# Kernel optimization log

Measured on AMD Instinct MI355X. Metric: run time of the kernel, lower is better.

The kernel has to match this reference:

```python
import jax, jax.numpy as jnp
import numpy as np

B, T, N, F, H, E = 8, 16, 10000, 64, 64, 1000000
M = B * N  # flattened node count per timestep
NUM_CLASSES = 3


def setup_inputs() -> dict:
    key = jax.random.key(0)
    ks = jax.random.split(key, 10)
    s = 1.0 / np.sqrt(H)
    return {
        "graph_seq": jax.random.normal(ks[0], (B, T, N, F), dtype=jnp.float32),
        "edge_index_seq": jax.random.randint(ks[1], (T, 2, E), 0, M, dtype=jnp.int32),
        "W_gcn": jax.random.normal(ks[2], (F, H), dtype=jnp.float32) / np.sqrt(F),
        "b_gcn": jnp.zeros((H,), dtype=jnp.float32),
        "W_ih": jax.random.uniform(ks[3], (4 * H, H), jnp.float32, -s, s),
        "W_hh": jax.random.uniform(ks[4], (4 * H, H), jnp.float32, -s, s),
        "b_ih": jax.random.uniform(ks[5], (4 * H,), jnp.float32, -s, s),
        "b_hh": jax.random.uniform(ks[6], (4 * H,), jnp.float32, -s, s),
        "W_fc": jax.random.uniform(ks[7], (NUM_CLASSES, H), jnp.float32, -s, s),
        "b_fc": jax.random.uniform(ks[8], (NUM_CLASSES,), jnp.float32, -s, s),
    }


def _forward(graph_seq, edge_index_seq, W_gcn, b_gcn, W_ih, W_hh, b_ih, b_hh, W_fc, b_fc):
    # GCNConv: x' = D^{-1/2}(A+I)D^{-1/2} (x W) + b, applied on flattened (B*N) nodes per timestep.
    xw = jnp.einsum('btnf,fh->btnh', graph_seq, W_gcn)        # [B,T,N,H]
    xw_t = xw.transpose(1, 0, 2, 3).reshape(T, M, H)          # [T, B*N, H], node index = b*N + n

    def gcn_step(_, inp):
        x, ei = inp                                           # x: [M,H], ei: [2,E]
        src, dst = ei[0], ei[1]
        deg = jax.ops.segment_sum(jnp.ones((E,), x.dtype), dst, num_segments=M) + 1.0  # +1 self loop
        dinv = jax.lax.rsqrt(deg)
        coef = dinv[src] * dinv[dst]                          # [E]
        agg = jax.ops.segment_sum(x[src] * coef[:, None], dst, num_segments=M)
        out = agg + x * (dinv * dinv)[:, None] + b_gcn        # self-loop term + bias
        pooled = out.reshape(B, N, H).mean(axis=1)            # mean over nodes -> [B,H]
        return None, pooled

    _, pooled_seq = jax.lax.scan(gcn_step, None, (xw_t, edge_index_seq))  # [T,B,H]

    def lstm_step(carry, x_t):
        h, c = carry
        z = x_t @ W_ih.T + h @ W_hh.T + b_ih + b_hh           # [B,4H], gate order i,f,g,o
        i, f, g, o = jnp.split(z, 4, axis=-1)
        c = jax.nn.sigmoid(f) * c + jax.nn.sigmoid(i) * jnp.tanh(g)
        h = jax.nn.sigmoid(o) * jnp.tanh(c)
        return (h, c), None

    h0 = jnp.zeros((B, H), dtype=graph_seq.dtype)
    (h_last, _), _ = jax.lax.scan(lstm_step, (h0, h0), pooled_seq)
    return h_last @ W_fc.T + b_fc                             # [B,3]


def reference(graph_seq, edge_index_seq, W_gcn, b_gcn, W_ih, W_hh, b_ih, b_hh, W_fc, b_fc):
    return _forward(graph_seq, edge_index_seq, W_gcn, b_gcn, W_ih, W_hh, b_ih, b_hh, W_fc, b_fc)
```

## Files before the change

kernel.cpp:

```cpp
#include <hip/hip_runtime.h>
#include <hip/hip_bf16.h>

#define BB 8
#define TT 16
#define NNODE 10000
#define FF 64
#define HH 64
#define EE 1000000
#define MM 80000
#define NCLS 3

#define NCHUNK 80
#define NPC 1000
#define NSEG_H 16
#define HW 20000
#define NSEG_B 32
#define NW 128
#define EPW 7816
#define WCAP 56
#define FLUSH_THR 32
#define RCAP 152

__global__ __launch_bounds__(256) void k_hist(const int* __restrict__ ei,
                                              unsigned int* __restrict__ part, int t0) {
    __shared__ unsigned int h[HW];
    int seg = blockIdx.x, tloc = blockIdx.y, tg = t0 + tloc;
    for (int i = threadIdx.x; i < HW; i += 256) h[i] = 0u;
    __syncthreads();
    const uint4* dstp = (const uint4*)(ei + (size_t)tg * 2 * EE + EE
                                       + (size_t)seg * (EE / NSEG_H));
    for (int i = threadIdx.x; i < (EE / NSEG_H) / 4; i += 256) {
        uint4 d4 = dstp[i];
        atomicAdd(&h[d4.x >> 2], 1u << ((d4.x & 3u) * 8u));
        atomicAdd(&h[d4.y >> 2], 1u << ((d4.y & 3u) * 8u));
        atomicAdd(&h[d4.z >> 2], 1u << ((d4.z & 3u) * 8u));
        atomicAdd(&h[d4.w >> 2], 1u << ((d4.w & 3u) * 8u));
    }
    __syncthreads();
    unsigned int* outp = part + ((size_t)tloc * NSEG_H + seg) * HW;
    for (int i = threadIdx.x; i < HW; i += 256) outp[i] = h[i];
}

__global__ __launch_bounds__(256) void k_mdeg(const unsigned int* __restrict__ part,
                                              unsigned int* __restrict__ degb) {
    int w = blockIdx.x * 256 + threadIdx.x;
    int tloc = blockIdx.y;
    if (w >= HW) return;
    const unsigned int* p = part + (size_t)tloc * NSEG_H * HW;
    unsigned int s = 0;
#pragma unroll
    for (int k = 0; k < NSEG_H; k++) s += p[(size_t)k * HW + w];
    degb[(size_t)tloc * HW + w] = s;
}

__global__ __launch_bounds__(256) void k_part(const int* __restrict__ ei,
                                              unsigned int* __restrict__ buck,
                                              unsigned int* __restrict__ hdr, int t0) {
    __shared__ unsigned int stg[4][NCHUNK][WCAP];
    __shared__ unsigned int cur[4][NCHUNK];
    __shared__ unsigned int gct[4][NCHUNK];
    int wave = threadIdx.x >> 6, lane = threadIdx.x & 63;
    int tloc = blockIdx.y, tg = t0 + tloc;
    if (lane < 64) { cur[wave][lane] = 0u; gct[wave][lane] = 0u; }
    if (lane < NCHUNK - 64) { cur[wave][64 + lane] = 0u; gct[wave][64 + lane] = 0u; }

    int wseg = blockIdx.x * 4 + wave;
    int e0 = wseg * EPW;
    int e1 = e0 + EPW; if (e1 > EE) e1 = EE;
    const uint4* src4 = (const uint4*)(ei + (size_t)tg * 2 * EE);
    const uint4* dst4 = (const uint4*)(ei + (size_t)tg * 2 * EE + EE);
    unsigned int* bkt = buck + ((size_t)tloc * NCHUNK * NW + wseg) * RCAP;

    int i40 = e0 >> 2, i41 = e1 >> 2;
    int nIter = (i41 - i40 + 63) >> 6;
    for (int k = 0; k < nIter; k++) {
        int i4 = i40 + k * 64 + lane;
        if (i4 < i41) {
            uint4 s4 = src4[i4];
            uint4 d4 = dst4[i4];
            unsigned int ss[4] = {s4.x, s4.y, s4.z, s4.w};
            unsigned int dd[4] = {d4.x, d4.y, d4.z, d4.w};
#pragma unroll
            for (int j = 0; j < 4; j++) {
                unsigned int ck = (unsigned int)(((unsigned long long)ss[j] * 4294968ull) >> 32);
                unsigned int so = ss[j] - ck * NPC;
                unsigned int p = atomicAdd(&cur[wave][ck], 1u);
                if (p < WCAP) stg[wave][ck][p] = (so << 17) | dd[j];
            }
        }
#pragma unroll
        for (int half = 0; half < 2; half++) {
            int nh = half ? (NCHUNK - 64) : 64;
            unsigned int cnt = (lane < nh) ? cur[wave][half * 64 + lane] : 0u;
            unsigned long long mask = __ballot(cnt >= FLUSH_THR);
            while (mask) {
                int ck = half * 64 + (__ffsll((unsigned long long)mask) - 1);
                mask &= mask - 1;
                unsigned int n = cur[wave][ck];
                if (n > WCAP) n = WCAP;
                unsigned int gp = gct[wave][ck];
                unsigned int nw = (gp + n <= RCAP) ? n : ((gp < RCAP) ? (RCAP - gp) : 0u);
                unsigned int* rg = bkt + (size_t)ck * NW * RCAP;
                if (lane < nw) rg[gp + lane] = stg[wave][ck][lane];
                if (lane == 0) { gct[wave][ck] = gp + nw; cur[wave][ck] = 0u; }
            }
        }
    }
    for (int ck = 0; ck < NCHUNK; ck++) {
        unsigned int n = cur[wave][ck];
        if (n > WCAP) n = WCAP;
        if (n > 0u) {
            unsigned int gp = gct[wave][ck];
            unsigned int nw = (gp + n <= RCAP) ? n : ((gp < RCAP) ? (RCAP - gp) : 0u);
            unsigned int* rg = bkt + (size_t)ck * NW * RCAP;
            if (lane < nw) rg[gp + lane] = stg[wave][ck][lane];
            if (lane == 0) gct[wave][ck] = gp + nw;
        }
    }
    for (int ck = lane; ck < NCHUNK; ck += 64)
        hdr[((size_t)tloc * NCHUNK + ck) * NW + wseg] = gct[wave][ck];
}

__global__ __launch_bounds__(512) void k_scat(const float* __restrict__ g,
                                              const unsigned int* __restrict__ degb,
                                              const unsigned int* __restrict__ buck,
                                              const unsigned int* __restrict__ hdr,
                                              float* __restrict__ yp, int t0) {
    __shared__ float a[NPC * BB];
    __shared__ float lut[256];
    __shared__ unsigned int hcnt[NW];
    int c = blockIdx.x, tloc = blockIdx.y, tg = t0 + tloc;
    int wave = threadIdx.x >> 6, lane = threadIdx.x & 63;

    for (int i = threadIdx.x; i < NPC * BB; i += 512) a[i] = 0.0f;
    if (threadIdx.x < 256) lut[threadIdx.x] = rsqrtf((float)threadIdx.x + 1.0f);
    if (threadIdx.x < NW)
        hcnt[threadIdx.x] = hdr[((size_t)tloc * NCHUNK + c) * NW + threadIdx.x];
    __syncthreads();

    const unsigned char* degc = (const unsigned char*)(degb + (size_t)tloc * HW);
    const unsigned int* bkc = buck + ((size_t)tloc * NCHUNK + c) * NW * RCAP;

    for (int r = wave; r < NW; r += 8) {
        unsigned int cnt = hcnt[r];
        if (cnt > RCAP) cnt = RCAP;
        const uint4* rg4 = (const uint4*)(bkc + (size_t)r * RCAP);
        unsigned int i0 = lane << 2;
        if (i0 < cnt) {
            uint4 rr = rg4[lane];
            unsigned int recs[4] = {rr.x, rr.y, rr.z, rr.w};
#pragma unroll
            for (int k = 0; k < 4; k++) {
                if (i0 + (unsigned)k < cnt) {
                    unsigned int rec = recs[k];
                    unsigned int d = rec & 0x1FFFFu;
                    unsigned int so = rec >> 17;
                    unsigned int b = (unsigned int)(((unsigned long long)d * 429497ull) >> 32);
                    atomicAdd(&a[so * BB + b], lut[degc[d]]);
                }
            }
        }
    }
    __syncthreads();

    int b_c = c / 10, coff = c - b_c * 10;
    int jbase = c * NPC;
    for (int j = threadIdx.x; j < NPC; j += 512) {
        float dvj = lut[degc[jbase + j]];
        float* aj = &a[j * BB];
#pragma unroll
        for (int b = 0; b < BB; b++)
            aj[b] = dvj * (aj[b] + (b == b_c ? dvj : 0.0f));
    }
    __syncthreads();

    int sub = lane >> 4;
    int f0 = (lane & 15) << 2;
    const float* gbase = g + ((size_t)(b_c * TT + tg) * NNODE + (size_t)coff * NPC) * FF;

    float acc[BB][4];
#pragma unroll
    for (int b = 0; b < BB; b++)
#pragma unroll
        for (int q = 0; q < 4; q++) acc[b][q] = 0.0f;

    const int NG = NPC / 4;
    for (int gi = wave; gi < NG; gi += 16) {
        int j0 = gi * 4 + sub;
        int gi1 = gi + 8;
        int j1 = gi1 * 4 + sub;
        bool h1 = (gi1 < NG);
        const float4 g40 = *(const float4*)(gbase + (size_t)j0 * FF + f0);
        float4 g41 = h1 ? *(const float4*)(gbase + (size_t)j1 * FF + f0)
                        : make_float4(0.f, 0.f, 0.f, 0.f);
        {
            const float4 a0 = *(const float4*)(&a[j0 * BB]);
            const float4 a1 = *(const float4*)(&a[j0 * BB + 4]);
            float av[BB] = {a0.x, a0.y, a0.z, a0.w, a1.x, a1.y, a1.z, a1.w};
#pragma unroll
            for (int b = 0; b < BB; b++) {
                acc[b][0] = fmaf(g40.x, av[b], acc[b][0]);
                acc[b][1] = fmaf(g40.y, av[b], acc[b][1]);
                acc[b][2] = fmaf(g40.z, av[b], acc[b][2]);
                acc[b][3] = fmaf(g40.w, av[b], acc[b][3]);
            }
        }
        if (h1) {
            const float4 a0 = *(const float4*)(&a[j1 * BB]);
            const float4 a1 = *(const float4*)(&a[j1 * BB + 4]);
            float av[BB] = {a0.x, a0.y, a0.z, a0.w, a1.x, a1.y, a1.z, a1.w};
#pragma unroll
            for (int b = 0; b < BB; b++) {
                acc[b][0] = fmaf(g41.x, av[b], acc[b][0]);
                acc[b][1] = fmaf(g41.y, av[b], acc[b][1]);
                acc[b][2] = fmaf(g41.z, av[b], acc[b][2]);
                acc[b][3] = fmaf(g41.w, av[b], acc[b][3]);
            }
        }
    }

    __syncthreads();
#pragma unroll
    for (int b = 0; b < BB; b++)
#pragma unroll
        for (int q = 0; q < 4; q++) {
            float v = acc[b][q];
            v += __shfl_xor(v, 16);
            v += __shfl_xor(v, 32);
            acc[b][q] = v;
        }
    if (sub == 0) {
#pragma unroll
        for (int b = 0; b < BB; b++)
#pragma unroll
            for (int q = 0; q < 4; q++)
                a[wave * (BB * FF) + b * FF + f0 + q] = acc[b][q];
    }
    __syncthreads();
    {
        int idx = threadIdx.x;
        float s = 0.0f;
#pragma unroll
        for (int w = 0; w < 8; w++) s += a[w * (BB * FF) + idx];
        yp[((size_t)tg * NCHUNK + c) * (BB * FF) + idx] = s;
    }
}

__global__ __launch_bounds__(512) void k_fold(const float* __restrict__ yp,
                                              float* __restrict__ y2) {
    int t = blockIdx.x;
    int idx = threadIdx.x;
    const float* p = yp + (size_t)t * NCHUNK * BB * FF + idx;
    float s = 0.0f;
#pragma unroll 8
    for (int u = 0; u < NCHUNK; u++) s += p[(size_t)u * BB * FF];
    y2[(size_t)t * BB * FF + idx] = s;
}

__global__ __launch_bounds__(256) void k_lstm(const float* __restrict__ y2,
                                              const float* __restrict__ Wg,
                                              const float* __restrict__ bg,
                                              const float* __restrict__ Wih,
                                              const float* __restrict__ Whh,
                                              const float* __restrict__ bih,
                                              const float* __restrict__ bhh,
                                              const float* __restrict__ Wfc,
                                              const float* __restrict__ bfc,
                                              float* __restrict__ out) {
    int b = blockIdx.x;
    int r = threadIdx.x;

    __shared__ float xs[TT][HH];
    __shared__ float hs[HH], cs[HH], zs[4 * HH];

    for (int idx = r; idx < TT * HH; idx += 256) {
        int t = idx >> 6, h = idx & 63;
        const float* yt = y2 + ((size_t)t * BB + b) * FF;
        float s = 0.0f;
#pragma unroll
        for (int f = 0; f < FF; f++) s = fmaf(yt[f], Wg[f * HH + h], s);
        xs[t][h] = s * (1.0f / NNODE) + bg[h];
    }

    float wih[HH], whh[HH];
#pragma unroll
    for (int k = 0; k < HH; k++) {
        wih[k] = Wih[r * HH + k];
        whh[k] = Whh[r * HH + k];
    }
    float bias = bih[r] + bhh[r];

    if (r < HH) { hs[r] = 0.0f; cs[r] = 0.0f; }
    __syncthreads();

    for (int t = 0; t < TT; t++) {
        float acc = bias;
#pragma unroll
        for (int k = 0; k < HH; k++)
            acc = fmaf(wih[k], xs[t][k], fmaf(whh[k], hs[k], acc));
        zs[r] = acc;
        __syncthreads();
        if (r < HH) {
            float iv = zs[r], fv = zs[HH + r], gv = zs[2 * HH + r], ov = zs[3 * HH + r];
            float si = 1.0f / (1.0f + expf(-iv));
            float sf = 1.0f / (1.0f + expf(-fv));
            float so = 1.0f / (1.0f + expf(-ov));
            float cc = sf * cs[r] + si * tanhf(gv);
            cs[r] = cc;
            hs[r] = so * tanhf(cc);
        }
        __syncthreads();
    }

    if (r < NCLS) {
        float s = bfc[r];
#pragma unroll
        for (int k = 0; k < HH; k++) s = fmaf(hs[k], Wfc[r * HH + k], s);
        out[b * NCLS + r] = s;
    }
}

extern "C" void kernel_launch(void* const* d_in, const int* in_sizes, int n_in,
                              void* d_out, int out_size, void* d_ws, size_t ws_size,
                              hipStream_t stream) {
    const float* g   = (const float*)d_in[0];
    const int*   ei  = (const int*)d_in[1];
    const float* Wg  = (const float*)d_in[2];
    const float* bg  = (const float*)d_in[3];
    const float* Wih = (const float*)d_in[4];
    const float* Whh = (const float*)d_in[5];
    const float* bih = (const float*)d_in[6];
    const float* bhh = (const float*)d_in[7];
    const float* Wfc = (const float*)d_in[8];
    const float* bfc = (const float*)d_in[9];
    float* out = (float*)d_out;

    char* ws = (char*)d_ws;
    float* yp = (float*)ws;
    const size_t ypBytes = (size_t)TT * NCHUNK * BB * FF * sizeof(float);
    float* y2 = (float*)(ws + ypBytes);
    const size_t y2Bytes = (size_t)TT * BB * FF * sizeof(float);
    const size_t headBytes = ypBytes + y2Bytes;

    const size_t sz_part = (size_t)NSEG_H * HW * 4;
    const size_t sz_degb = (size_t)HW * 4;
    const size_t sz_buck = (size_t)NCHUNK * NW * RCAP * 4;
    const size_t sz_hdr  = (size_t)NCHUNK * NW * 4;
    const size_t per_t = sz_part + sz_degb + sz_buck + sz_hdr;

    size_t avail = (ws_size > headBytes) ? ws_size - headBytes : 0;
    int Tg = (int)(avail / per_t);
    if (Tg > TT) Tg = TT;
    if (Tg < 1) Tg = 1;

    size_t ofs = headBytes;
    unsigned int* part = (unsigned int*)(ws + ofs); ofs += (size_t)Tg * sz_part;
    unsigned int* degb = (unsigned int*)(ws + ofs); ofs += (size_t)Tg * sz_degb;
    unsigned int* hdr  = (unsigned int*)(ws + ofs); ofs += (size_t)Tg * sz_hdr;
    unsigned int* buck = (unsigned int*)(ws + ofs);

    for (int t0 = 0; t0 < TT; t0 += Tg) {
        int tc = (TT - t0 < Tg) ? (TT - t0) : Tg;

        dim3 gh(NSEG_H, tc);
        k_hist<<<gh, 256, 0, stream>>>(ei, part, t0);

        dim3 gm((HW + 255) / 256, tc);
        k_mdeg<<<gm, 256, 0, stream>>>(part, degb);

        dim3 gp(NSEG_B, tc);
        k_part<<<gp, 256, 0, stream>>>(ei, buck, hdr, t0);

        dim3 gs(NCHUNK, tc);
        k_scat<<<gs, 512, 0, stream>>>(g, degb, buck, hdr, yp, t0);
    }

    k_fold<<<TT, 512, 0, stream>>>(yp, y2);
    k_lstm<<<BB, 256, 0, stream>>>(y2, Wg, bg, Wih, Whh, bih, bhh, Wfc, bfc, out);
}
```

Before: 313.3 us.

## Software-pipeline scatter and GEMV across four chunks per block with double buffering

Result: slower. 385.9 us (+23.2%).

```diff
diff --git a/kernel.cpp b/kernel.cpp
--- a/kernel.cpp
+++ b/kernel.cpp
@@ -20,6 +20,7 @@
 #define WCAP 56
 #define FLUSH_THR 32
 #define RCAP 152
+#define NCPB 4
 
 __global__ __launch_bounds__(256) void k_hist(const int* __restrict__ ei,
                                               unsigned int* __restrict__ part, int t0) {
@@ -126,124 +127,152 @@
                                               const unsigned int* __restrict__ buck,
                                               const unsigned int* __restrict__ hdr,
                                               float* __restrict__ yp, int t0) {
-    __shared__ float a[NPC * BB];
-    __shared__ float lut[256];
-    __shared__ unsigned int hcnt[NW];
-    int c = blockIdx.x, tloc = blockIdx.y, tg = t0 + tloc;
+    __shared__ float buf[2][NPC * BB];
+    __shared__ unsigned int hcA[NCPB][NW];
+    int c0 = blockIdx.x * NCPB, tloc = blockIdx.y, tg = t0 + tloc;
     int wave = threadIdx.x >> 6, lane = threadIdx.x & 63;
 
-    for (int i = threadIdx.x; i < NPC * BB; i += 512) a[i] = 0.0f;
-    if (threadIdx.x < 256) lut[threadIdx.x] = rsqrtf((float)threadIdx.x + 1.0f);
-    if (threadIdx.x < NW)
-        hcnt[threadIdx.x] = hdr[((size_t)tloc * NCHUNK + c) * NW + threadIdx.x];
+    for (int i = threadIdx.x; i < NPC * BB; i += 512) { buf[0][i] = 0.0f; buf[1][i] = 0.0f; }
+    {
+        int j = threadIdx.x >> 7;
+        int r = threadIdx.x & 127;
+        hcA[j][r] = hdr[((size_t)tloc * NCHUNK + (c0 + j)) * NW + r];
+    }
     __syncthreads();
 
     const unsigned char* degc = (const unsigned char*)(degb + (size_t)tloc * HW);
-    const unsigned int* bkc = buck + ((size_t)tloc * NCHUNK + c) * NW * RCAP;
-
-    for (int r = wave; r < NW; r += 8) {
-        unsigned int cnt = hcnt[r];
-        if (cnt > RCAP) cnt = RCAP;
-        const uint4* rg4 = (const uint4*)(bkc + (size_t)r * RCAP);
-        unsigned int i0 = lane << 2;
-        if (i0 < cnt) {
-            uint4 rr = rg4[lane];
-            unsigned int recs[4] = {rr.x, rr.y, rr.z, rr.w};
-#pragma unroll
-            for (int k = 0; k < 4; k++) {
-                if (i0 + (unsigned)k < cnt) {
-                    unsigned int rec = recs[k];
-                    unsigned int d = rec & 0x1FFFFu;
-                    unsigned int so = rec >> 17;
-                    unsigned int b = (unsigned int)(((unsigned long long)d * 429497ull) >> 32);
-                    atomicAdd(&a[so * BB + b], lut[degc[d]]);
+
+#define BUILD_REGION(j, t, r)                                                    \
+    {                                                                            \
+        const unsigned int* bkc_ = buck + ((size_t)tloc * NCHUNK + (c0 + (j))) * NW * RCAP; \
+        unsigned int cnt = hcA[(j)][(r)];                                        \
+        if (cnt > RCAP) cnt = RCAP;                                              \
+        const uint4* rg4 = (const uint4*)(bkc_ + (size_t)(r) * RCAP);            \
+        unsigned int i0 = lane << 2;                                             \
+        if (i0 < cnt) {                                                          \
+            uint4 rr = rg4[lane];                                                \
+            unsigned int rrs[4] = {rr.x, rr.y, rr.z, rr.w};                      \
+            _Pragma("unroll")                                                    \
+            for (int k = 0; k < 4; k++) {                                        \
+                if (i0 + (unsigned)k < cnt) {                                    \
+                    unsigned int rec = rrs[k];                                   \
+                    unsigned int d = rec & 0x1FFFFu;                             \
+                    unsigned int so = rec >> 17;                                 \
+                    unsigned int b = (unsigned int)(((unsigned long long)d * 429497ull) >> 32); \
+                    float dv = rsqrtf((float)degc[d] + 1.0f);                    \
+                    atomicAdd(&buf[t][so * BB + b], dv);                         \
+                }                                                                \
+            }                                                                    \
+        }                                                                        \
+    }
+
+#define PREFOLD(j, t)                                                            \
+    {                                                                            \
+        int bc_ = (c0 + (j)) / 10;                                               \
+        int jb_ = (c0 + (j)) * NPC;                                              \
+        for (int jj = threadIdx.x; jj < NPC; jj += 512) {                        \
+            float dvj = rsqrtf((float)degc[jb_ + jj] + 1.0f);                    \
+            float* aj = &buf[t][jj * BB];                                        \
+            _Pragma("unroll")                                                    \
+            for (int b = 0; b < BB; b++)                                         \
+                aj[b] = dvj * (aj[b] + (b == bc_ ? dvj : 0.0f));                 \
+        }                                                                        \
+    }
+
+    for (int step = 0; step < 16; step++) BUILD_REGION(0, 0, step * 8 + wave);
+    __syncthreads();
+    PREFOLD(0, 0);
+    __syncthreads();
+
+    int sub = lane >> 4;
+    int f0 = (lane & 15) << 2;
+    const int NG = NPC / 4;
+
+    for (int i = 0; i < NCPB; i++) {
+        int p = i & 1, q = p ^ 1;
+        int c = c0 + i;
+        int b_c = c / 10, coff = c - b_c * 10;
+        const float* gbase = g + ((size_t)(b_c * TT + tg) * NNODE + (size_t)coff * NPC) * FF;
+        bool hasB = (i + 1 < NCPB);
+
+        float acc[BB][4];
+#pragma unroll
+        for (int b = 0; b < BB; b++)
+#pragma unroll
+            for (int qq = 0; qq < 4; qq++) acc[b][qq] = 0.0f;
+
+        for (int step = 0; step < 16; step++) {
+            int gi = wave + step * 16;
+            int j0 = gi * 4 + sub;
+            int gi1 = gi + 8;
+            int j1 = gi1 * 4 + sub;
+            bool h1 = (gi1 < NG);
+            const float4 g40 = *(const float4*)(gbase + (size_t)j0 * FF + f0);
+            float4 g41 = h1 ? *(const float4*)(gbase + (size_t)j1 * FF + f0)
+                            : make_float4(0.f, 0.f, 0.f, 0.f);
+            if (hasB) BUILD_REGION(i + 1, q, step * 8 + wave);
+            {
+                const float4 a0 = *(const float4*)(&buf[p][j0 * BB]);
+                const float4 a1 = *(const float4*)(&buf[p][j0 * BB + 4]);
+                float av[BB] = {a0.x, a0.y, a0.z, a0.w, a1.x, a1.y, a1.z, a1.w};
+#pragma unroll
+                for (int b = 0; b < BB; b++) {
+                    acc[b][0] = fmaf(g40.x, av[b], acc[b][0]);
+                    acc[b][1] = fmaf(g40.y, av[b], acc[b][1]);
+                    acc[b][2] = fmaf(g40.z, av[b], acc[b][2]);
+                    acc[b][3] = fmaf(g40.w, av[b], acc[b][3]);
                 }
             }
-        }
-    }
-    __syncthreads();
-
-    int b_c = c / 10, coff = c - b_c * 10;
-    int jbase = c * NPC;
-    for (int j = threadIdx.x; j < NPC; j += 512) {
-        float dvj = lut[degc[jbase + j]];
-        float* aj = &a[j * BB];
+            if (h1) {
+                const float4 a0 = *(const float4*)(&buf[p][j1 * BB]);
+                const float4 a1 = *(const float4*)(&buf[p][j1 * BB + 4]);
+                float av[BB] = {a0.x, a0.y, a0.z, a0.w, a1.x, a1.y, a1.z, a1.w};
+#pragma unroll
+                for (int b = 0; b < BB; b++) {
+                    acc[b][0] = fmaf(g41.x, av[b], acc[b][0]);
+                    acc[b][1] = fmaf(g41.y, av[b], acc[b][1]);
+                    acc[b][2] = fmaf(g41.z, av[b], acc[b][2]);
+                    acc[b][3] = fmaf(g41.w, av[b], acc[b][3]);
+                }
+            }
+        }
+        __syncthreads();
+
 #pragma unroll
         for (int b = 0; b < BB; b++)
-            aj[b] = dvj * (aj[b] + (b == b_c ? dvj : 0.0f));
-    }
-    __syncthreads();
-
-    int sub = lane >> 4;
-    int f0 = (lane & 15) << 2;
-    const float* gbase = g + ((size_t)(b_c * TT + tg) * NNODE + (size_t)coff * NPC) * FF;
-
-    float acc[BB][4];
-#pragma unroll
-    for (int b = 0; b < BB; b++)
-#pragma unroll
-        for (int q = 0; q < 4; q++) acc[b][q] = 0.0f;
-
-    const int NG = NPC / 4;
-    for (int gi = wave; gi < NG; gi += 16) {
-        int j0 = gi * 4 + sub;
-        int gi1 = gi + 8;
-        int j1 = gi1 * 4 + sub;
-        bool h1 = (gi1 < NG);
-        const float4 g40 = *(const float4*)(gbase + (size_t)j0 * FF + f0);
-        float4 g41 = h1 ? *(const float4*)(gbase + (size_t)j1 * FF + f0)
-                        : make_float4(0.f, 0.f, 0.f, 0.f);
+#pragma unroll
+            for (int qq = 0; qq < 4; qq++) {
+                float v = acc[b][qq];
+                v += __shfl_xor(v, 16);
+                v += __shfl_xor(v, 32);
+                acc[b][qq] = v;
+            }
+        if (sub == 0) {
+#pragma unroll
+            for (int b = 0; b < BB; b++)
+#pragma unroll
+                for (int qq = 0; qq < 4; qq++)
+                    buf[p][wave * (BB * FF) + b * FF + f0 + qq] = acc[b][qq];
+        }
+        if (hasB) PREFOLD(i + 1, q);
+        __syncthreads();
+
         {
-            const float4 a0 = *(const float4*)(&a[j0 * BB]);
-            const float4 a1 = *(const float4*)(&a[j0 * BB + 4]);
-            float av[BB] = {a0.x, a0.y, a0.z, a0.w, a1.x, a1.y, a1.z, a1.w};
-#pragma unroll
-            for (int b = 0; b < BB; b++) {
-                acc[b][0] = fmaf(g40.x, av[b], acc[b][0]);
-                acc[b][1] = fmaf(g40.y, av[b], acc[b][1]);
-                acc[b][2] = fmaf(g40.z, av[b], acc[b][2]);
-                acc[b][3] = fmaf(g40.w, av[b], acc[b][3]);
-            }
-        }
-        if (h1) {
-            const float4 a0 = *(const float4*)(&a[j1 * BB]);
-            const float4 a1 = *(const float4*)(&a[j1 * BB + 4]);
-            float av[BB] = {a0.x, a0.y, a0.z, a0.w, a1.x, a1.y, a1.z, a1.w};
-#pragma unroll
-            for (int b = 0; b < BB; b++) {
-                acc[b][0] = fmaf(g41.x, av[b], acc[b][0]);
-                acc[b][1] = fmaf(g41.y, av[b], acc[b][1]);
-                acc[b][2] = fmaf(g41.z, av[b], acc[b][2]);
-                acc[b][3] = fmaf(g41.w, av[b], acc[b][3]);
-            }
-        }
-    }
-
-    __syncthreads();
-#pragma unroll
-    for (int b = 0; b < BB; b++)
-#pragma unroll
-        for (int q = 0; q < 4; q++) {
-            float v = acc[b][q];
-            v += __shfl_xor(v, 16);
-            v += __shfl_xor(v, 32);
-            acc[b][q] = v;
-        }
-    if (sub == 0) {
-#pragma unroll
-        for (int b = 0; b < BB; b++)
-#pragma unroll
-            for (int q = 0; q < 4; q++)
-                a[wave * (BB * FF) + b * FF + f0 + q] = acc[b][q];
-    }
-    __syncthreads();
-    {
-        int idx = threadIdx.x;
-        float s = 0.0f;
-#pragma unroll
-        for (int w = 0; w < 8; w++) s += a[w * (BB * FF) + idx];
-        yp[((size_t)tg * NCHUNK + c) * (BB * FF) + idx] = s;
-    }
+            int idx = threadIdx.x;
+            float s = 0.0f;
+#pragma unroll
+            for (int w = 0; w < 8; w++) s += buf[p][w * (BB * FF) + idx];
+            yp[((size_t)tg * NCHUNK + c) * (BB * FF) + idx] = s;
+        }
+        __syncthreads();
+
+        if (i + 2 < NCPB) {
+            for (int k2 = threadIdx.x; k2 < NPC * BB; k2 += 512) buf[p][k2] = 0.0f;
+            __syncthreads();
+        }
+    }
+#undef BUILD_REGION
+#undef PREFOLD
 }
 
 __global__ __launch_bounds__(512) void k_fold(const float* __restrict__ yp,
@@ -371,7 +400,7 @@
         dim3 gp(NSEG_B, tc);
         k_part<<<gp, 256, 0, stream>>>(ei, buck, hdr, t0);
 
-        dim3 gs(NCHUNK, tc);
+        dim3 gs(NCHUNK / NCPB, tc);
         k_scat<<<gs, 512, 0, stream>>>(g, degb, buck, hdr, yp, t0);
     }
 
```
